# Kernel tuning notes

Measured on AMD Instinct MI355X. Metric: run time of the kernel, lower is better.

## Reference

```python
import jax, jax.numpy as jnp
import numpy as np

N, G, K, D = 16, 4096, 8, 2  # agents, grid points (64x64 flattened), fiber dim, manifold dim


def setup_inputs() -> dict:
    key = jax.random.key(0)
    k0, k1, k2, k3 = jax.random.split(key, 4)
    I = jnp.eye(K, dtype=jnp.float32)
    # frames and links: identity + small perturbation (invertible, as init_twist_scale=0.05 implies)
    omega = I + 0.05 * jax.random.normal(k0, (N, G, K, K), dtype=jnp.float32)
    links = I + 0.05 * jax.random.normal(k1, (N, D, G, K, K), dtype=jnp.float32)
    mu_q = jax.random.normal(k2, (N, G, K), dtype=jnp.float32)
    A = 0.3 * jax.random.normal(k3, (N, G, K, K), dtype=jnp.float32)
    sigma_q = A @ A.swapaxes(-1, -2) + I  # SPD covariances
    return {"omega": omega, "links": links, "mu_q": mu_q, "sigma_q": sigma_q}


def reference(omega, links, mu_q, sigma_q):
    """pairwise_alignment_with_twists: E[i,j,g] = KL(q_i || Omega_ij[q_j]).

    full_transport: Omega_ij = omega_i @ V_i @ inv(omega_j),
    V_i = I + sum_d (link_{i,d} - I)   (links depend only on i, per source).
    """
    I = jnp.eye(K, dtype=omega.dtype)
    V = I + jnp.sum(links - I, axis=1)                       # (N,G,K,K)
    T = omega @ V                                            # omega_i V_i, (N,G,K,K)
    omega_inv = jnp.linalg.inv(omega)                        # (N,G,K,K)
    Om = jnp.einsum('igab,jgbc->ijgac', T, omega_inv)        # (N,N,G,K,K)

    mu_t = jnp.einsum('ijgab,jgb->ijga', Om, mu_q)           # transported means
    sig_t = jnp.einsum('ijgab,jgbc,ijgdc->ijgad', Om, sigma_q, Om)  # Om Sigma Om^T

    inv2 = jnp.linalg.inv(sig_t)                             # Sigma2^{-1}
    diff = mu_t - mu_q[:, None]                              # (N,N,G,K)
    tr = jnp.einsum('ijgab,igba->ijg', inv2, sigma_q)        # tr(Sigma2^{-1} Sigma1)
    quad = jnp.einsum('ijga,ijgab,ijgb->ijg', diff, inv2, diff)
    ld2 = jnp.linalg.slogdet(sig_t)[1]                       # (N,N,G)
    ld1 = jnp.linalg.slogdet(sigma_q)[1]                     # (N,G)
    E = 0.5 * (tr + quad - K + ld2 - ld1[:, None, :])
    # zero the diagonal (i == j skipped in the original loop)
    mask = 1.0 - jnp.eye(N, dtype=E.dtype)
    return E * mask[:, :, None]
```

## Files before the change

kernel.cpp:

```cpp
#include <hip/hip_runtime.h>
#include <math.h>

#define NN 16
#define GG 4096
#define GP 2
#define STR 76
#define NWG (GG / GP)

template <int CTRL>
__device__ __forceinline__ float dppf(float x) {
    return __builtin_bit_cast(float, __builtin_amdgcn_mov_dpp(
        __builtin_bit_cast(int, x), CTRL, 0xF, 0xF, true));
}
__device__ __forceinline__ float qb(float x, int L) {
    switch (L) {
        case 0:  return dppf<0x00>(x);
        case 1:  return dppf<0x55>(x);
        case 2:  return dppf<0xAA>(x);
        default: return dppf<0xFF>(x);
    }
}
__device__ __forceinline__ float qsum(float x) {
    x += dppf<0xB1>(x);
    x += dppf<0x4E>(x);
    return x;
}
__device__ __forceinline__ void bcast_row(float out[8], const float r0[8],
                                          const float r1[8], int k) {
#pragma unroll
    for (int c = 0; c < 8; ++c) {
        float s = (k < 4) ? r0[c] : r1[c];
        out[c] = qb(s, k & 3);
    }
}
__device__ __forceinline__ float sel_lo(const float r[8], int q) {
    return (q == 0) ? r[0] : (q == 1) ? r[1] : (q == 2) ? r[2] : r[3];
}
__device__ __forceinline__ float sel_hi(const float r[8], int q) {
    return (q == 0) ? r[4] : (q == 1) ? r[5] : (q == 2) ? r[6] : r[7];
}
__device__ __forceinline__ void ld_row(float r[8], const float* p) {
    float4 x = *(const float4*)p, y = *(const float4*)(p + 4);
    r[0] = x.x; r[1] = x.y; r[2] = x.z; r[3] = x.w;
    r[4] = y.x; r[5] = y.y; r[6] = y.z; r[7] = y.w;
}
__device__ __forceinline__ void st_row(float* p, const float r[8]) {
    *(float4*)p       = make_float4(r[0], r[1], r[2], r[3]);
    *(float4*)(p + 4) = make_float4(r[4], r[5], r[6], r[7]);
}
__device__ __forceinline__ float dot8(const float a[8], const float b[8]) {
    float s = a[0] * b[0];
    s = fmaf(a[1], b[1], s); s = fmaf(a[2], b[2], s);
    s = fmaf(a[3], b[3], s); s = fmaf(a[4], b[4], s);
    s = fmaf(a[5], b[5], s); s = fmaf(a[6], b[6], s);
    s = fmaf(a[7], b[7], s);
    return s;
}

__device__ __forceinline__ float gj4(float r0[8], float r1[8], int q) {
    float pp = 1.0f;
#pragma unroll
    for (int k = 0; k < 8; ++k) {
        float Mk[8];
        bcast_row(Mk, r0, r1, k);
        float p = Mk[k];
        pp *= p;
        float ip = 1.0f / p;
        bool own0 = (k < 4) && (q == k);
        bool own1 = (k >= 4) && (q == k - 4);
        float m0 = -(own0 ? -1.0f : r0[k]) * ip;
        float m1 = -(own1 ? -1.0f : r1[k]) * ip;
#pragma unroll
        for (int c = 0; c < 8; ++c) {
            float b0 = own0 ? 0.0f : r0[c];
            float b1 = own1 ? 0.0f : r1[c];
            r0[c] = fmaf(m0, Mk[c], b0);
            r1[c] = fmaf(m1, Mk[c], b1);
        }
        r0[k] = m0;
        r1[k] = m1;
    }
    return pp;
}

__global__ __launch_bounds__(256) void pairkl_kernel(
    const float* __restrict__ omega, const float* __restrict__ links,
    const float* __restrict__ mu, const float* __restrict__ sigma,
    float* __restrict__ out) {
    __shared__ __align__(16) float sh_om[GP][NN][STR];
    __shared__ __align__(16) float sh_sg[GP][NN][STR];
    __shared__ __align__(16) float sh_wv[GP][NN][STR];
    __shared__ __align__(16) float sh_mu[GP][NN][8];
    __shared__ float sh_ld1[GP][NN];
#define sh_x sh_wv
#define sh_y sh_om

    const int bid  = blockIdx.x;
    const int work = (bid & 7) * (NWG / 8) + (bid >> 3);
    const int g0   = work * GP;
    const int t    = threadIdx.x;

    {
        const int gl = t >> 7, s = t & 127;
        const int g  = g0 + gl;
        const float4* om4 = (const float4*)omega;
        const float4* sg4 = (const float4*)sigma;
        const float4* lk4 = (const float4*)links;
#pragma unroll
        for (int k = 0; k < 2; ++k) {
            int fc = s + 128 * k;
            int i = fc >> 4, qq = fc & 15;
            int b4 = (i * GG + g) * 16 + qq;
            float4 o  = om4[b4];
            float4 sv = sg4[b4];
            float4 l0 = lk4[((i * 2 + 0) * GG + g) * 16 + qq];
            float4 l1 = lk4[((i * 2 + 1) * GG + g) * 16 + qq];
            float4 v = make_float4(l0.x + l1.x, l0.y + l1.y, l0.z + l1.z, l0.w + l1.w);
            int e0 = qq * 4;
            if (((e0 + 0) >> 3) == ((e0 + 0) & 7)) v.x -= 1.f;
            if (((e0 + 1) >> 3) == ((e0 + 1) & 7)) v.y -= 1.f;
            if (((e0 + 2) >> 3) == ((e0 + 2) & 7)) v.z -= 1.f;
            if (((e0 + 3) >> 3) == ((e0 + 3) & 7)) v.w -= 1.f;
            *(float4*)&sh_om[gl][i][e0] = o;
            *(float4*)&sh_sg[gl][i][e0] = sv;
            *(float4*)&sh_wv[gl][i][e0] = v;
        }
        if (t < 64) {
            int gl2 = t >> 5, mi = (t >> 1) & 15, h = t & 1;
            const float4* mu4 = (const float4*)mu;
            *(float4*)&sh_mu[gl2][mi][h * 4] = mu4[(mi * GG + g0 + gl2) * 2 + h];
        }
    }
    __syncthreads();

    const int wid  = t >> 6;
    const int gl   = wid & 1;
    const int isB  = wid >> 1;
    const int lane = t & 63;
    const int item = lane >> 2;
    const int q    = lane & 3;

    float R0[8], R1[8];
    float mq[8];
    ld_row(mq, &sh_mu[gl][item][0]);

    float ldT = 0.f, ld1B = 0.f, ldoB = 0.f, ccB = 0.f;

    if (!isB) {
        float o0[8], o1[8];
        ld_row(o0, &sh_om[gl][item][q * 8]);
        ld_row(o1, &sh_om[gl][item][(q + 4) * 8]);
#pragma unroll
        for (int c = 0; c < 8; ++c) { R0[c] = 0.f; R1[c] = 0.f; }
        const float* vv = &sh_wv[gl][item][0];
#pragma unroll
        for (int b = 0; b < 8; ++b) {
            float vr[8]; ld_row(vr, vv + b * 8);
#pragma unroll
            for (int c = 0; c < 8; ++c) {
                R0[c] = fmaf(o0[b], vr[c], R0[c]);
                R1[c] = fmaf(o1[b], vr[c], R1[c]);
            }
        }
        float ppT = gj4(R0, R1, q);
        ldT = logf(fabsf(ppT));
    } else {
        float a0[8], a1[8];
        ld_row(a0, &sh_om[gl][item][q * 8]);
        ld_row(a1, &sh_om[gl][item][(q + 4) * 8]);
        float ppo = gj4(a0, a1, q);
        ld_row(R0, &sh_sg[gl][item][q * 8]);
        ld_row(R1, &sh_sg[gl][item][(q + 4) * 8]);
        float pps = gj4(R0, R1, q);
        float cq = dot8(R0, mq) * sel_lo(mq, q) + dot8(R1, mq) * sel_hi(mq, q);
        ccB  = qsum(cq);
        ld1B = logf(fabsf(pps));
        ldoB = logf(fabsf(ppo));
        if (q == 0) sh_ld1[gl][item] = ld1B;
    }
    __syncthreads();

    if (!isB) {
        float u_lo = dot8(R0, mq), u_hi = dot8(R1, mq);
        float uf[8];
#pragma unroll
        for (int c = 0; c < 4; ++c) { uf[c] = qb(u_lo, c); uf[c + 4] = qb(u_hi, c); }
        float Z0[8], Z1[8];
#pragma unroll
        for (int c = 0; c < 8; ++c) { Z0[c] = 0.f; Z1[c] = 0.f; }
        const float* sg = &sh_sg[gl][item][0];
#pragma unroll
        for (int b = 0; b < 8; ++b) {
            float sr[8]; ld_row(sr, sg + b * 8);
#pragma unroll
            for (int c = 0; c < 8; ++c) {
                Z0[c] = fmaf(R0[b], sr[c], Z0[c]);
                Z1[c] = fmaf(R1[b], sr[c], Z1[c]);
            }
        }
        float X0[8], X1[8];
#pragma unroll
        for (int c = 0; c < 8; ++c) {
            float Wc[8]; bcast_row(Wc, R0, R1, c);
            X0[c] = fmaf(u_lo, uf[c], dot8(Z0, Wc));
            X1[c] = fmaf(u_hi, uf[c], dot8(Z1, Wc));
        }
        st_row(&sh_x[gl][item][q * 8], X0);
        st_row(&sh_x[gl][item][(q + 4) * 8], X1);
        if (q == 0) {
            float ld1 = sh_ld1[gl][item];
            float a_i = 2.f * ldT - ld1;
            *(float4*)&sh_x[gl][item][64] = make_float4(uf[0], uf[1], uf[2], uf[3]);
            *(float4*)&sh_x[gl][item][68] = make_float4(uf[4], uf[5], uf[6], uf[7]);
            *(float4*)&sh_x[gl][item][72] = make_float4(a_i, 1.f, 0.f, 0.f);
        }
    } else {
        float S0[8], S1[8], oq[8], oq4[8];
#pragma unroll
        for (int c = 0; c < 8; ++c) { S0[c] = 0.f; S1[c] = 0.f; }
        const float* om = &sh_om[gl][item][0];
#pragma unroll
        for (int b = 0; b < 8; ++b) {
            float orow[8]; ld_row(orow, om + b * 8);
#pragma unroll
            for (int c = 0; c < 8; ++c) {
                S0[c] = fmaf(R0[b], orow[c], S0[c]);
                S1[c] = fmaf(R1[b], orow[c], S1[c]);
            }
            oq[b]  = sel_lo(orow, q);
            oq4[b] = sel_hi(orow, q);
        }
        float P0[8], P1[8];
#pragma unroll
        for (int c = 0; c < 8; ++c) { P0[c] = 0.f; P1[c] = 0.f; }
#pragma unroll
        for (int a = 0; a < 8; ++a) {
            float Sa[8]; bcast_row(Sa, S0, S1, a);
#pragma unroll
            for (int c = 0; c < 8; ++c) {
                P0[c] = fmaf(oq[a],  Sa[c], P0[c]);
                P1[c] = fmaf(oq4[a], Sa[c], P1[c]);
            }
        }
        float wp[8];
        {
            float mlo = sel_lo(mq, q), mhi = sel_hi(mq, q);
#pragma unroll
            for (int c = 0; c < 8; ++c)
                wp[c] = qsum(fmaf(mlo, S0[c], mhi * S1[c]));
        }
        st_row(&sh_y[gl][item][q * 8], P0);
        st_row(&sh_y[gl][item][(q + 4) * 8], P1);
        if (q == 0) {
            float s_j = ld1B - 2.f * ldoB + ccB - 8.0f;
            *(float4*)&sh_y[gl][item][64] =
                make_float4(-2.f * wp[0], -2.f * wp[1], -2.f * wp[2], -2.f * wp[3]);
            *(float4*)&sh_y[gl][item][68] =
                make_float4(-2.f * wp[4], -2.f * wp[5], -2.f * wp[6], -2.f * wp[7]);
            *(float4*)&sh_y[gl][item][72] = make_float4(1.f, s_j, 0.f, 0.f);
        }
    }
    __syncthreads();

    if (t < 128) {
        const int gl2 = t >> 6, r = t & 63;
        const int i0 = r >> 3, j0 = r & 7;
        const int i1 = i0 + 8, j1 = j0 + 8;
        const float4* x0 = (const float4*)&sh_x[gl2][i0][0];
        const float4* x1 = (const float4*)&sh_x[gl2][i1][0];
        const float4* y0 = (const float4*)&sh_y[gl2][j0][0];
        const float4* y1 = (const float4*)&sh_y[gl2][j1][0];
        float d00 = 0.f, d01 = 0.f, d10 = 0.f, d11 = 0.f;
#pragma unroll
        for (int k = 0; k < STR / 4; ++k) {
            float4 a0 = x0[k], a1 = x1[k], b0 = y0[k], b1 = y1[k];
            d00 = fmaf(a0.x, b0.x, d00); d00 = fmaf(a0.y, b0.y, d00);
            d00 = fmaf(a0.z, b0.z, d00); d00 = fmaf(a0.w, b0.w, d00);
            d01 = fmaf(a0.x, b1.x, d01); d01 = fmaf(a0.y, b1.y, d01);
            d01 = fmaf(a0.z, b1.z, d01); d01 = fmaf(a0.w, b1.w, d01);
            d10 = fmaf(a1.x, b0.x, d10); d10 = fmaf(a1.y, b0.y, d10);
            d10 = fmaf(a1.z, b0.z, d10); d10 = fmaf(a1.w, b0.w, d10);
            d11 = fmaf(a1.x, b1.x, d11); d11 = fmaf(a1.y, b1.y, d11);
            d11 = fmaf(a1.z, b1.z, d11); d11 = fmaf(a1.w, b1.w, d11);
        }
        const int g = g0 + gl2;
        const bool dg = (i0 == j0);
        out[(i0 * NN + j0) * GG + g] = dg ? 0.f : 0.5f * d00;
        out[(i0 * NN + j1) * GG + g] = 0.5f * d01;
        out[(i1 * NN + j0) * GG + g] = 0.5f * d10;
        out[(i1 * NN + j1) * GG + g] = dg ? 0.f : 0.5f * d11;
    }
}

extern "C" void kernel_launch(void* const* d_in, const int* in_sizes, int n_in,
                              void* d_out, int out_size, void* d_ws, size_t ws_size,
                              hipStream_t stream) {
    const float* omega = (const float*)d_in[0];
    const float* links = (const float*)d_in[1];
    const float* mu    = (const float*)d_in[2];
    const float* sigma = (const float*)d_in[3];
    float* out = (float*)d_out;
    hipLaunchKernelGGL(pairkl_kernel, dim3(NWG), dim3(256), 0, stream,
                       omega, links, mu, sigma, out);
}
```

Before: 29.53 us.

## Load operands directly from global into registers, drop staging barrier

Removes the shared-memory staging of omega, sigma, links and mu and one block barrier. Each wave now loads its own rows straight from global memory into registers and uses cross-lane broadcasts instead of shared-memory row reads. The B wave's P computation is reordered around a t1 = omega^T-row times sigma intermediate. The ld1 term moves from the A side to the B side through a separate x/y column. This removes a barrier and shared traffic, but both waves now load omega and sigma redundantly and the global loads are less coalesced.

```diff
diff --git a/kernel.cpp b/kernel.cpp
--- a/kernel.cpp
+++ b/kernel.cpp
@@ -87,117 +87,73 @@
     const float* __restrict__ omega, const float* __restrict__ links,
     const float* __restrict__ mu, const float* __restrict__ sigma,
     float* __restrict__ out) {
-    __shared__ __align__(16) float sh_om[GP][NN][STR];
-    __shared__ __align__(16) float sh_sg[GP][NN][STR];
-    __shared__ __align__(16) float sh_wv[GP][NN][STR];
-    __shared__ __align__(16) float sh_mu[GP][NN][8];
-    __shared__ float sh_ld1[GP][NN];
-#define sh_x sh_wv
-#define sh_y sh_om
+    __shared__ __align__(16) float sh_x[GP][NN][STR];
+    __shared__ __align__(16) float sh_y[GP][NN][STR];
 
     const int bid  = blockIdx.x;
     const int work = (bid & 7) * (NWG / 8) + (bid >> 3);
     const int g0   = work * GP;
     const int t    = threadIdx.x;
-
-    {
-        const int gl = t >> 7, s = t & 127;
-        const int g  = g0 + gl;
-        const float4* om4 = (const float4*)omega;
-        const float4* sg4 = (const float4*)sigma;
-        const float4* lk4 = (const float4*)links;
-#pragma unroll
-        for (int k = 0; k < 2; ++k) {
-            int fc = s + 128 * k;
-            int i = fc >> 4, qq = fc & 15;
-            int b4 = (i * GG + g) * 16 + qq;
-            float4 o  = om4[b4];
-            float4 sv = sg4[b4];
-            float4 l0 = lk4[((i * 2 + 0) * GG + g) * 16 + qq];
-            float4 l1 = lk4[((i * 2 + 1) * GG + g) * 16 + qq];
-            float4 v = make_float4(l0.x + l1.x, l0.y + l1.y, l0.z + l1.z, l0.w + l1.w);
-            int e0 = qq * 4;
-            if (((e0 + 0) >> 3) == ((e0 + 0) & 7)) v.x -= 1.f;
-            if (((e0 + 1) >> 3) == ((e0 + 1) & 7)) v.y -= 1.f;
-            if (((e0 + 2) >> 3) == ((e0 + 2) & 7)) v.z -= 1.f;
-            if (((e0 + 3) >> 3) == ((e0 + 3) & 7)) v.w -= 1.f;
-            *(float4*)&sh_om[gl][i][e0] = o;
-            *(float4*)&sh_sg[gl][i][e0] = sv;
-            *(float4*)&sh_wv[gl][i][e0] = v;
-        }
-        if (t < 64) {
-            int gl2 = t >> 5, mi = (t >> 1) & 15, h = t & 1;
-            const float4* mu4 = (const float4*)mu;
-            *(float4*)&sh_mu[gl2][mi][h * 4] = mu4[(mi * GG + g0 + gl2) * 2 + h];
-        }
-    }
-    __syncthreads();
-
     const int wid  = t >> 6;
     const int gl   = wid & 1;
     const int isB  = wid >> 1;
     const int lane = t & 63;
     const int item = lane >> 2;
     const int q    = lane & 3;
-
-    float R0[8], R1[8];
-    float mq[8];
-    ld_row(mq, &sh_mu[gl][item][0]);
-
-    float ldT = 0.f, ld1B = 0.f, ldoB = 0.f, ccB = 0.f;
+    const int g    = g0 + gl;
+    const int mb   = (item * GG + g) * 64;
 
     if (!isB) {
-        float o0[8], o1[8];
-        ld_row(o0, &sh_om[gl][item][q * 8]);
-        ld_row(o1, &sh_om[gl][item][(q + 4) * 8]);
+        float v0[8], v1[8], o0[8], o1[8], s0[8], s1[8], mq[8];
+        {
+            const float* l0p = links + ((item * 2 + 0) * GG + g) * 64;
+            const float* l1p = links + ((item * 2 + 1) * GG + g) * 64;
+            float la[8], lb[8];
+            ld_row(la, l0p + q * 8);
+            ld_row(lb, l1p + q * 8);
+#pragma unroll
+            for (int c = 0; c < 8; ++c)
+                v0[c] = la[c] + lb[c] - ((c == q) ? 1.f : 0.f);
+            ld_row(la, l0p + (q + 4) * 8);
+            ld_row(lb, l1p + (q + 4) * 8);
+#pragma unroll
+            for (int c = 0; c < 8; ++c)
+                v1[c] = la[c] + lb[c] - ((c == q + 4) ? 1.f : 0.f);
+        }
+        ld_row(o0, omega + mb + q * 8);
+        ld_row(o1, omega + mb + (q + 4) * 8);
+        ld_row(s0, sigma + mb + q * 8);
+        ld_row(s1, sigma + mb + (q + 4) * 8);
+        ld_row(mq, mu + (item * GG + g) * 8);
+        float R0[8], R1[8];
 #pragma unroll
         for (int c = 0; c < 8; ++c) { R0[c] = 0.f; R1[c] = 0.f; }
-        const float* vv = &sh_wv[gl][item][0];
 #pragma unroll
         for (int b = 0; b < 8; ++b) {
-            float vr[8]; ld_row(vr, vv + b * 8);
-#pragma unroll
-            for (int c = 0; c < 8; ++c) {
-                R0[c] = fmaf(o0[b], vr[c], R0[c]);
-                R1[c] = fmaf(o1[b], vr[c], R1[c]);
-            }
-        }
-        float ppT = gj4(R0, R1, q);
-        ldT = logf(fabsf(ppT));
-    } else {
-        float a0[8], a1[8];
-        ld_row(a0, &sh_om[gl][item][q * 8]);
-        ld_row(a1, &sh_om[gl][item][(q + 4) * 8]);
-        float ppo = gj4(a0, a1, q);
-        ld_row(R0, &sh_sg[gl][item][q * 8]);
-        ld_row(R1, &sh_sg[gl][item][(q + 4) * 8]);
-        float pps = gj4(R0, R1, q);
-        float cq = dot8(R0, mq) * sel_lo(mq, q) + dot8(R1, mq) * sel_hi(mq, q);
-        ccB  = qsum(cq);
-        ld1B = logf(fabsf(pps));
-        ldoB = logf(fabsf(ppo));
-        if (q == 0) sh_ld1[gl][item] = ld1B;
-    }
-    __syncthreads();
-
-    if (!isB) {
+            float Vb[8]; bcast_row(Vb, v0, v1, b);
+#pragma unroll
+            for (int c = 0; c < 8; ++c) {
+                R0[c] = fmaf(o0[b], Vb[c], R0[c]);
+                R1[c] = fmaf(o1[b], Vb[c], R1[c]);
+            }
+        }
+        float ldT = logf(fabsf(gj4(R0, R1, q)));
+        float Z0[8], Z1[8];
+#pragma unroll
+        for (int c = 0; c < 8; ++c) { Z0[c] = 0.f; Z1[c] = 0.f; }
+#pragma unroll
+        for (int b = 0; b < 8; ++b) {
+            float Sb[8]; bcast_row(Sb, s0, s1, b);
+#pragma unroll
+            for (int c = 0; c < 8; ++c) {
+                Z0[c] = fmaf(R0[b], Sb[c], Z0[c]);
+                Z1[c] = fmaf(R1[b], Sb[c], Z1[c]);
+            }
+        }
         float u_lo = dot8(R0, mq), u_hi = dot8(R1, mq);
         float uf[8];
 #pragma unroll
         for (int c = 0; c < 4; ++c) { uf[c] = qb(u_lo, c); uf[c + 4] = qb(u_hi, c); }
-        float Z0[8], Z1[8];
-#pragma unroll
-        for (int c = 0; c < 8; ++c) { Z0[c] = 0.f; Z1[c] = 0.f; }
-        const float* sg = &sh_sg[gl][item][0];
-#pragma unroll
-        for (int b = 0; b < 8; ++b) {
-            float sr[8]; ld_row(sr, sg + b * 8);
-#pragma unroll
-            for (int c = 0; c < 8; ++c) {
-                Z0[c] = fmaf(R0[b], sr[c], Z0[c]);
-                Z1[c] = fmaf(R1[b], sr[c], Z1[c]);
-            }
-        }
         float X0[8], X1[8];
 #pragma unroll
         for (int c = 0; c < 8; ++c) {
@@ -208,56 +164,61 @@
         st_row(&sh_x[gl][item][q * 8], X0);
         st_row(&sh_x[gl][item][(q + 4) * 8], X1);
         if (q == 0) {
-            float ld1 = sh_ld1[gl][item];
-            float a_i = 2.f * ldT - ld1;
             *(float4*)&sh_x[gl][item][64] = make_float4(uf[0], uf[1], uf[2], uf[3]);
             *(float4*)&sh_x[gl][item][68] = make_float4(uf[4], uf[5], uf[6], uf[7]);
-            *(float4*)&sh_x[gl][item][72] = make_float4(a_i, 1.f, 0.f, 0.f);
+            *(float2*)&sh_x[gl][item][72] = make_float2(2.f * ldT, 1.f);
         }
     } else {
-        float S0[8], S1[8], oq[8], oq4[8];
-#pragma unroll
-        for (int c = 0; c < 8; ++c) { S0[c] = 0.f; S1[c] = 0.f; }
-        const float* om = &sh_om[gl][item][0];
+        float o0[8], o1[8], s0[8], s1[8], mq[8];
+        ld_row(o0, omega + mb + q * 8);
+        ld_row(o1, omega + mb + (q + 4) * 8);
+        ld_row(s0, sigma + mb + q * 8);
+        ld_row(s1, sigma + mb + (q + 4) * 8);
+        ld_row(mq, mu + (item * GG + g) * 8);
+        float ld1 = logf(fabsf(gj4(s0, s1, q)));
+        float cc  = qsum(dot8(s0, mq) * sel_lo(mq, q) +
+                         dot8(s1, mq) * sel_hi(mq, q));
+        if (q == 0) *(float2*)&sh_x[gl][item][74] = make_float2(-ld1, 0.f);
+        float t10[8], t11[8];
+#pragma unroll
+        for (int c = 0; c < 8; ++c) { t10[c] = 0.f; t11[c] = 0.f; }
+#pragma unroll
+        for (int a = 0; a < 8; ++a) {
+            float Oa[8]; bcast_row(Oa, o0, o1, a);
+            float Sa[8]; bcast_row(Sa, s0, s1, a);
+            float oqa = sel_lo(Oa, q), oqa4 = sel_hi(Oa, q);
+#pragma unroll
+            for (int c = 0; c < 8; ++c) {
+                t10[c] = fmaf(oqa,  Sa[c], t10[c]);
+                t11[c] = fmaf(oqa4, Sa[c], t11[c]);
+            }
+        }
+        float w_lo = dot8(t10, mq), w_hi = dot8(t11, mq);
+        float wf[8];
+#pragma unroll
+        for (int c = 0; c < 4; ++c) { wf[c] = qb(w_lo, c); wf[c + 4] = qb(w_hi, c); }
+        float P0[8], P1[8];
+#pragma unroll
+        for (int c = 0; c < 8; ++c) { P0[c] = 0.f; P1[c] = 0.f; }
 #pragma unroll
         for (int b = 0; b < 8; ++b) {
-            float orow[8]; ld_row(orow, om + b * 8);
-#pragma unroll
-            for (int c = 0; c < 8; ++c) {
-                S0[c] = fmaf(R0[b], orow[c], S0[c]);
-                S1[c] = fmaf(R1[b], orow[c], S1[c]);
-            }
-            oq[b]  = sel_lo(orow, q);
-            oq4[b] = sel_hi(orow, q);
-        }
-        float P0[8], P1[8];
-#pragma unroll
-        for (int c = 0; c < 8; ++c) { P0[c] = 0.f; P1[c] = 0.f; }
-#pragma unroll
-        for (int a = 0; a < 8; ++a) {
-            float Sa[8]; bcast_row(Sa, S0, S1, a);
-#pragma unroll
-            for (int c = 0; c < 8; ++c) {
-                P0[c] = fmaf(oq[a],  Sa[c], P0[c]);
-                P1[c] = fmaf(oq4[a], Sa[c], P1[c]);
-            }
-        }
-        float wp[8];
-        {
-            float mlo = sel_lo(mq, q), mhi = sel_hi(mq, q);
-#pragma unroll
-            for (int c = 0; c < 8; ++c)
-                wp[c] = qsum(fmaf(mlo, S0[c], mhi * S1[c]));
+            float Ob[8]; bcast_row(Ob, o0, o1, b);
+#pragma unroll
+            for (int c = 0; c < 8; ++c) {
+                P0[c] = fmaf(t10[b], Ob[c], P0[c]);
+                P1[c] = fmaf(t11[b], Ob[c], P1[c]);
+            }
         }
         st_row(&sh_y[gl][item][q * 8], P0);
         st_row(&sh_y[gl][item][(q + 4) * 8], P1);
+        float ldo = logf(fabsf(gj4(o0, o1, q)));
         if (q == 0) {
-            float s_j = ld1B - 2.f * ldoB + ccB - 8.0f;
+            float s_j = ld1 - 2.f * ldo + cc - 8.0f;
             *(float4*)&sh_y[gl][item][64] =
-                make_float4(-2.f * wp[0], -2.f * wp[1], -2.f * wp[2], -2.f * wp[3]);
+                make_float4(-2.f * wf[0], -2.f * wf[1], -2.f * wf[2], -2.f * wf[3]);
             *(float4*)&sh_y[gl][item][68] =
-                make_float4(-2.f * wp[4], -2.f * wp[5], -2.f * wp[6], -2.f * wp[7]);
-            *(float4*)&sh_y[gl][item][72] = make_float4(1.f, s_j, 0.f, 0.f);
+                make_float4(-2.f * wf[4], -2.f * wf[5], -2.f * wf[6], -2.f * wf[7]);
+            *(float4*)&sh_y[gl][item][72] = make_float4(1.f, s_j, 1.f, 0.f);
         }
     }
     __syncthreads();
@@ -283,12 +244,12 @@
             d11 = fmaf(a1.x, b1.x, d11); d11 = fmaf(a1.y, b1.y, d11);
             d11 = fmaf(a1.z, b1.z, d11); d11 = fmaf(a1.w, b1.w, d11);
         }
-        const int g = g0 + gl2;
+        const int gg = g0 + gl2;
         const bool dg = (i0 == j0);
-        out[(i0 * NN + j0) * GG + g] = dg ? 0.f : 0.5f * d00;
-        out[(i0 * NN + j1) * GG + g] = 0.5f * d01;
-        out[(i1 * NN + j0) * GG + g] = 0.5f * d10;
-        out[(i1 * NN + j1) * GG + g] = dg ? 0.f : 0.5f * d11;
+        out[(i0 * NN + j0) * GG + gg] = dg ? 0.f : 0.5f * d00;
+        out[(i0 * NN + j1) * GG + gg] = 0.5f * d01;
+        out[(i1 * NN + j0) * GG + gg] = 0.5f * d10;
+        out[(i1 * NN + j1) * GG + gg] = dg ? 0.f : 0.5f * d11;
     }
 }
 
```

Result: faster. 26.96 us (-8.7%).
